# Kernel optimization log

Measured on AMD Instinct MI355X. Metric: run time of the kernel, lower is better.

## Reference

```python
import jax, jax.numpy as jnp
import numpy as np

B, L, C, H, V = 64, 512, 256, 4, 32000
D = C // H
DIL = (1, 2, 4)
WIN = 3
NC = (50, 20)
NEG = -1e9


def setup_inputs() -> dict:
    key = jax.random.key(0)
    ks = jax.random.split(key, 20)
    g = lambda i, shape: jax.random.normal(ks[i], shape, jnp.float32) * 0.05
    Lay = len(DIL)
    x = jax.random.randint(ks[0], (B, L), 0, V)
    emb = g(1, (V, C)).at[0].set(0.0)  # padding_idx=0 row is zero
    return dict(
        x=x, emb=emb, pos=g(2, (L, C)),
        gp_W=g(3, (Lay, C, C)), gp_as=g(4, (Lay, H, D)), gp_ad=g(5, (Lay, H, D)),
        gf_W=g(6, (Lay, C, C)), gf_as=g(7, (Lay, H, D)), gf_ad=g(8, (Lay, H, D)),
        msg_W=g(9, (Lay, C, 2 * C)), msg_b=jnp.zeros((Lay, C), jnp.float32),
        gru_Wih=g(10, (Lay, 3 * C, C)), gru_bih=jnp.zeros((Lay, 3 * C), jnp.float32),
        gru_Whh=g(11, (Lay, 3 * C, C)), gru_bhh=jnp.zeros((Lay, 3 * C), jnp.float32),
        ln_g=jnp.ones((Lay, C), jnp.float32), ln_b=jnp.zeros((Lay, C), jnp.float32),
        pool_w=g(12, (C,)), pool_b=jnp.zeros((), jnp.float32),
        h0_W=g(13, (NC[0], C)), h0_b=jnp.zeros((NC[0],), jnp.float32),
        h1_W=g(14, (NC[1], C)), h1_b=jnp.zeros((NC[1],), jnp.float32),
    )


def _dense_gat(x, W, a_src, a_dst, adj):
    # x: [B,L,C], W: [C_out,C_in], a_*: [H,D], adj: [B,L,L] bool
    b, l, _ = x.shape
    h = jnp.einsum('blc,oc->blo', x, W).reshape(b, l, H, D).transpose(0, 2, 1, 3)  # [B,H,L,D]
    s = jnp.einsum('bhld,hd->bhl', h, a_src)
    d = jnp.einsum('bhld,hd->bhl', h, a_dst)
    e = s[:, :, :, None] + d[:, :, None, :]            # [B,H,L,L]
    e = jnp.where(e > 0, e, 0.2 * e)                   # LeakyReLU(0.2)
    e = jnp.where(adj[:, None, :, :], e, NEG)
    alpha = jax.nn.softmax(e, axis=-1)                 # dropout is identity in eval
    out = jnp.einsum('bhij,bhjd->bhid', alpha, h)
    return out.transpose(0, 2, 1, 3).reshape(b, l, C)


def _forward(x, emb, pos, gp_W, gp_as, gp_ad, gf_W, gf_as, gf_ad,
             msg_W, msg_b, gru_Wih, gru_bih, gru_Whh, gru_bhh,
             ln_g, ln_b, pool_w, pool_b, h0_W, h0_b, h1_W, h1_b):
    mask = x != 0                                      # [B,L]
    mf = mask.astype(jnp.float32)[..., None]           # [B,L,1]
    h = (emb[x] + pos[None, :, :] * mf) * mf
    logical = jnp.clip(jnp.cumsum(mask.astype(jnp.int32), axis=1) - 1, 0)
    valid = mask[:, None, :] & mask[:, :, None]        # [B,L,L]
    eye = jnp.eye(L, dtype=bool)[None]
    for l in range(len(DIL)):
        dil = DIL[l]
        diff = logical[:, :, None] - logical[:, None, :]
        ad = jnp.abs(diff)
        in_win = (ad <= WIN * dil) & (ad % dil == 0)
        adj_p = (valid & in_win & (diff < 0)) | eye
        adj_f = (valid & in_win & (diff > 0)) | eye
        m_p = _dense_gat(h, gp_W[l], gp_as[l], gp_ad[l], adj_p)
        m_f = _dense_gat(h, gf_W[l], gf_as[l], gf_ad[l], adj_f)
        m = jnp.concatenate([m_p, m_f], axis=-1)
        m = jax.nn.relu(jnp.einsum('blk,ck->blc', m, msg_W[l]) + msg_b[l])
        # GRUCell(input=m, hidden=h), PyTorch gate order: r,z,n
        gi = jnp.einsum('blc,gc->blg', m, gru_Wih[l]) + gru_bih[l]
        gh = jnp.einsum('blc,gc->blg', h, gru_Whh[l]) + gru_bhh[l]
        ir, iz, inn = jnp.split(gi, 3, axis=-1)
        hr, hz, hn = jnp.split(gh, 3, axis=-1)
        r = jax.nn.sigmoid(ir + hr)
        z = jax.nn.sigmoid(iz + hz)
        n = jnp.tanh(inn + r * hn)
        h_new = (1.0 - z) * n + z * h
        mu = jnp.mean(h_new, axis=-1, keepdims=True)
        var = jnp.mean(jnp.square(h_new - mu), axis=-1, keepdims=True)
        h_new = (h_new - mu) * jax.lax.rsqrt(var + 1e-5) * ln_g[l] + ln_b[l]
        h = h_new * mf
    # attention pooling over sequence (masked softmax on linear scores)
    sc = jnp.einsum('blc,c->bl', h, pool_w) + pool_b
    sc = jnp.where(mask, sc, NEG)
    a = jax.nn.softmax(sc, axis=-1)
    pooled = jnp.einsum('bl,blc->bc', a, h)            # dropout identity in eval
    o0 = pooled @ h0_W.T + h0_b
    o1 = pooled @ h1_W.T + h1_b
    return jnp.concatenate([o0, o1], axis=-1)          # [B, 50+20]


def reference(x, emb, pos, gp_W, gp_as, gp_ad, gf_W, gf_as, gf_ad,
              msg_W, msg_b, gru_Wih, gru_bih, gru_Whh, gru_bhh,
              ln_g, ln_b, pool_w, pool_b, h0_W, h0_b, h1_W, h1_b):
    return _forward(x, emb, pos, gp_W, gp_as, gp_ad, gf_W, gf_as, gf_ad,
                    msg_W, msg_b, gru_Wih, gru_bih, gru_Whh, gru_bhh,
                    ln_g, ln_b, pool_w, pool_b, h0_W, h0_b, h1_W, h1_b)
```

## Files before the change

kernel.cpp:

```cpp
#include <hip/hip_runtime.h>
#include <math.h>

#define B_ 64
#define L_ 512
#define C_ 256
#define H_ 4
#define LAY 3
#define NEGV -1e9f

#define GF_BIAS  1
#define GF_RELU  2
#define GF_OBF16 4

typedef __attribute__((ext_vector_type(8))) short short8;
typedef __attribute__((ext_vector_type(4))) short short4v;
typedef __attribute__((ext_vector_type(4))) float floatx4;

static __device__ __forceinline__ float rcp_(float x) { return __builtin_amdgcn_rcpf(x); }
static __device__ __forceinline__ float sig_(float x) { return rcp_(1.f + __expf(-x)); }
static __device__ __forceinline__ float tanh_(float x) {
    float e = __expf(2.f * x);
    return 1.f - 2.f * rcp_(e + 1.f);
}

static __device__ __forceinline__ short f2bf(float f) {
    unsigned x = __float_as_uint(f);
    x += 0x7fffu + ((x >> 16) & 1u);
    return (short)(x >> 16);
}
static __device__ __forceinline__ float bf2f(short s) {
    return __uint_as_float(((unsigned)(unsigned short)s) << 16);
}

static __device__ __forceinline__ int tok_swizzle(int blk) {
    int c8 = blk & 7, i = blk >> 3;
    return (c8 + 8 * (i >> 5)) * 128 + (i & 31) * 4;
}

static __device__ __forceinline__ void gl_lds16(const short* g, short* l) {
    __builtin_amdgcn_global_load_lds(
        (const __attribute__((address_space(1))) unsigned int*)g,
        (__attribute__((address_space(3))) unsigned int*)l, 16, 0, 0);
}

__global__ void scan_kernel(const int* __restrict__ x, int* __restrict__ mask,
                            int* __restrict__ logical, int* __restrict__ pol,
                            int* __restrict__ nvalid) {
    int b = blockIdx.x, t = threadIdx.x;
    __shared__ int s[L_];
    int m = (x[b * L_ + t] != 0) ? 1 : 0;
    s[t] = m;
    __syncthreads();
    for (int off = 1; off < L_; off <<= 1) {
        int v = (t >= off) ? s[t - off] : 0;
        __syncthreads();
        s[t] += v;
        __syncthreads();
    }
    int cum = s[t];
    int lg = cum - 1; if (lg < 0) lg = 0;
    mask[b * L_ + t] = m;
    logical[b * L_ + t] = lg;
    if (m) pol[b * L_ + lg] = t;
    if (t == L_ - 1) nvalid[b] = cum;
}

__global__ void embed_kernel(const int* __restrict__ x, const float* __restrict__ emb,
                             const float* __restrict__ pos, short* __restrict__ hb) {
    int t = threadIdx.x;
    int bl = tok_swizzle(blockIdx.x) + (t >> 6);
    int lane = t & 63;
    int xv = x[bl];
    float mf = (xv != 0) ? 1.f : 0.f;
    int l = bl & (L_ - 1);
    float4 e = *(const float4*)&emb[(size_t)xv * C_ + lane * 4];
    float4 p = *(const float4*)&pos[(size_t)l * C_ + lane * 4];
    short4v hv4;
    hv4.x = f2bf((e.x + p.x * mf) * mf);
    hv4.y = f2bf((e.y + p.y * mf) * mf);
    hv4.z = f2bf((e.z + p.z * mf) * mf);
    hv4.w = f2bf((e.w + p.w * mf) * mf);
    *(short4v*)&hb[(size_t)bl * C_ + lane * 4] = hv4;
}

__global__ void f2bf_kernel(const float* __restrict__ s, short* __restrict__ d, int n) {
    int i = blockIdx.x * 256 + threadIdx.x;
    if (i < n) d[i] = f2bf(s[i]);
}

__global__ void prep_wcomb(const float* __restrict__ gpW, const float* __restrict__ gfW,
                           const float* __restrict__ gpas, const float* __restrict__ gpad,
                           const float* __restrict__ gfas, const float* __restrict__ gfad,
                           short* __restrict__ Wc) {
    int i = blockIdx.x * 256 + threadIdx.x;
    if (i >= 3 * 640 * 256) return;
    int k = i & 255;
    int r = (i >> 8) % 640;
    int l = i / (640 * 256);
    float v = 0.f;
    if (r < 256) {
        v = gpW[((size_t)l * 256 + r) * 256 + k];
    } else if (r < 512) {
        v = gfW[((size_t)l * 256 + (r - 256)) * 256 + k];
    } else {
        int n = r - 512;
        if (n < 16) {
            int type = n >> 3, dir = (n >> 2) & 1, hh = n & 3;
            const float* a = type ? (dir ? gfad : gpad) : (dir ? gfas : gpas);
            const float* W = dir ? gfW : gpW;
            for (int j = 0; j < 64; j++) {
                float av = a[l * 256 + hh * 64 + j];
                float wv = W[((size_t)l * 256 + hh * 64 + j) * 256 + k];
                v = fmaf(av, wv, v);
            }
        }
    }
    Wc[i] = f2bf(v);
}

__global__ void prep_gru_i(const float* __restrict__ Wih, const float* __restrict__ Whh,
                           short* __restrict__ Bc) {
    int i = blockIdx.x * 256 + threadIdx.x;
    if (i >= 3 * 1024 * 512) return;
    int k = i & 511, np = (i >> 9) & 1023, l = i >> 19;
    int ch = np >> 2, g = np & 3;
    float v = 0.f;
    if (g < 2) {
        v = (k < 256) ? Wih[((size_t)l * 768 + g * 256 + ch) * 256 + k]
                      : Whh[((size_t)l * 768 + g * 256 + ch) * 256 + (k - 256)];
    } else if (g == 2) {
        if (k < 256) v = Wih[((size_t)l * 768 + 512 + ch) * 256 + k];
    } else {
        if (k >= 256) v = Whh[((size_t)l * 768 + 512 + ch) * 256 + (k - 256)];
    }
    Bc[i] = f2bf(v);
}

__global__ void prep_bias4(const float* __restrict__ bih, const float* __restrict__ bhh,
                           float* __restrict__ bc) {
    int i = blockIdx.x * 256 + threadIdx.x;
    if (i >= 3 * 1024) return;
    int np = i & 1023, l = i >> 10;
    int ch = np >> 2, g = np & 3;
    float v;
    if (g < 2)       v = bih[l * 768 + g * 256 + ch] + bhh[l * 768 + g * 256 + ch];
    else if (g == 2) v = bih[l * 768 + 512 + ch];
    else             v = bhh[l * 768 + 512 + ch];
    bc[i] = v;
}

__global__ __launch_bounds__(256) void bgemm(const short* __restrict__ A0,
                                             const short* __restrict__ Bw,
                                             void* __restrict__ Cout,
                                             const float* __restrict__ bias,
                                             int K, int lda, int ldc, int nstore,
                                             int cbBits, int flags) {
    __shared__ short As[128 * 32];
    __shared__ short Bs[128 * 32];
    const int id = blockIdx.x;
    const int cb = (id >> 3) & ((1 << cbBits) - 1);
    const int rb = (id & 7) + ((id >> (3 + cbBits)) << 3);
    const int tid = threadIdx.x;
    const int wave = tid >> 6, lane = tid & 63;
    const int wm = wave >> 1, wn = wave & 1;
    const size_t arow0 = (size_t)rb * 128;
    const short* Bb = Bw + (size_t)cb * 128 * K;
    floatx4 acc[4][4];
#pragma unroll
    for (int i = 0; i < 4; i++)
#pragma unroll
        for (int j = 0; j < 4; j++) acc[i][j] = (floatx4)0.f;

    const int srow = lane >> 2;
    const int sq = (lane & 3) * 8;
    const int q = lane >> 4, t16 = lane & 15;

    for (int k0 = 0; k0 < K; k0 += 32) {
        const short* Abase = A0 + arow0 * (size_t)lda + k0;
#pragma unroll
        for (int t = 0; t < 2; ++t) {
            int r = (wave * 2 + t) * 16 + srow;
            gl_lds16(Abase + (size_t)r * lda + sq, &As[r * 32 + sq]);
            gl_lds16(Bb + (size_t)r * K + k0 + sq, &Bs[r * 32 + sq]);
        }
        __syncthreads();
        short8 af[4], bfr[4];
#pragma unroll
        for (int mf = 0; mf < 4; mf++)
            af[mf] = *(const short8*)&As[(wm * 64 + mf * 16 + t16) * 32 + q * 8];
#pragma unroll
        for (int nf = 0; nf < 4; nf++)
            bfr[nf] = *(const short8*)&Bs[(wn * 64 + nf * 16 + t16) * 32 + q * 8];
#pragma unroll
        for (int mf = 0; mf < 4; mf++)
#pragma unroll
            for (int nf = 0; nf < 4; nf++)
                acc[nf][mf] = __builtin_amdgcn_mfma_f32_16x16x32_bf16(
                    bfr[nf], af[mf], acc[nf][mf], 0, 0, 0);
        __syncthreads();
    }

    const int rowbase = rb * 128 + wm * 64;
    const int colbase = cb * 128 + wn * 64;
#pragma unroll
    for (int nf = 0; nf < 4; nf++) {
        int col0 = colbase + nf * 16 + q * 4;
        if (col0 >= nstore) continue;
        float4 bv4 = make_float4(0.f, 0.f, 0.f, 0.f);
        if (flags & GF_BIAS) bv4 = *(const float4*)&bias[col0];
#pragma unroll
        for (int mf = 0; mf < 4; mf++) {
            int row = rowbase + mf * 16 + t16;
            float v0 = acc[nf][mf][0] + bv4.x;
            float v1 = acc[nf][mf][1] + bv4.y;
            float v2 = acc[nf][mf][2] + bv4.z;
            float v3 = acc[nf][mf][3] + bv4.w;
            if (flags & GF_RELU) {
                v0 = fmaxf(v0, 0.f); v1 = fmaxf(v1, 0.f);
                v2 = fmaxf(v2, 0.f); v3 = fmaxf(v3, 0.f);
            }
            size_t base = (size_t)row * ldc + col0;
            if (flags & GF_OBF16) {
                short4v pk;
                pk.x = f2bf(v0); pk.y = f2bf(v1); pk.z = f2bf(v2); pk.w = f2bf(v3);
                *(short4v*)&((short*)Cout)[base] = pk;
            } else {
                float4 pk = make_float4(v0, v1, v2, v3);
                *(float4*)&((float*)Cout)[base] = pk;
            }
        }
    }
}

__global__ __launch_bounds__(256) void projssd_bgemm(const short* __restrict__ A0,
                                                     const short* __restrict__ Bw,
                                                     short* __restrict__ hpb2,
                                                     float* __restrict__ Ssd) {
    __shared__ short As[128 * 32];
    __shared__ short Bs[128 * 32];
    const int id = blockIdx.x;
    const int grp = id >> 3;
    const int cb = grp % 5;
    const int rb = (id & 7) + (grp / 5) * 8;
    const int tid = threadIdx.x;
    const int wave = tid >> 6, lane = tid & 63;
    const int wm = wave >> 1, wn = wave & 1;
    const size_t arow0 = (size_t)rb * 128;
    const short* Bb = Bw + (size_t)cb * 128 * 256;
    floatx4 acc[4][4];
#pragma unroll
    for (int i = 0; i < 4; i++)
#pragma unroll
        for (int j = 0; j < 4; j++) acc[i][j] = (floatx4)0.f;

    const int srow = lane >> 2;
    const int sq = (lane & 3) * 8;
    const int q = lane >> 4, t16 = lane & 15;

    for (int k0 = 0; k0 < 256; k0 += 32) {
        const short* Abase = A0 + arow0 * 256 + k0;
#pragma unroll
        for (int t = 0; t < 2; ++t) {
            int r = (wave * 2 + t) * 16 + srow;
            gl_lds16(Abase + (size_t)r * 256 + sq, &As[r * 32 + sq]);
            gl_lds16(Bb + (size_t)r * 256 + k0 + sq, &Bs[r * 32 + sq]);
        }
        __syncthreads();
        short8 af[4], bfr[4];
#pragma unroll
        for (int mf = 0; mf < 4; mf++)
            af[mf] = *(const short8*)&As[(wm * 64 + mf * 16 + t16) * 32 + q * 8];
#pragma unroll
        for (int nf = 0; nf < 4; nf++)
            bfr[nf] = *(const short8*)&Bs[(wn * 64 + nf * 16 + t16) * 32 + q * 8];
#pragma unroll
        for (int mf = 0; mf < 4; mf++)
#pragma unroll
            for (int nf = 0; nf < 4; nf++)
                acc[nf][mf] = __builtin_amdgcn_mfma_f32_16x16x32_bf16(
                    bfr[nf], af[mf], acc[nf][mf], 0, 0, 0);
        __syncthreads();
    }

    const int rowbase = rb * 128 + wm * 64;
    if (cb < 4) {
        const int colbase = cb * 128 + wn * 64;
#pragma unroll
        for (int nf = 0; nf < 4; nf++) {
            int col0 = colbase + nf * 16 + q * 4;
#pragma unroll
            for (int mf = 0; mf < 4; mf++) {
                int row = rowbase + mf * 16 + t16;
                short4v pk;
                pk.x = f2bf(acc[nf][mf][0]);
                pk.y = f2bf(acc[nf][mf][1]);
                pk.z = f2bf(acc[nf][mf][2]);
                pk.w = f2bf(acc[nf][mf][3]);
                *(short4v*)&hpb2[(size_t)row * 512 + col0] = pk;
            }
        }
    } else {
        if (wn == 0) {
            int col0 = q * 4;
            if (col0 < 16) {
#pragma unroll
                for (int mf = 0; mf < 4; mf++) {
                    int row = rowbase + mf * 16 + t16;
                    float4 pk = make_float4(acc[0][mf][0], acc[0][mf][1],
                                            acc[0][mf][2], acc[0][mf][3]);
                    *(float4*)&Ssd[(size_t)row * 16 + col0] = pk;
                }
            }
        }
    }
}

__global__ __launch_bounds__(256) void gru_bgemm(const short* __restrict__ mmb,
                                                 const short* __restrict__ hb_in,
                                                 const short* __restrict__ Bw,
                                                 short* __restrict__ hn2b,
                                                 const float* __restrict__ bias4) {
    __shared__ short As[128 * 36];
    __shared__ short Bs[128 * 32];
    const int id = blockIdx.x;
    const int cb = (id >> 3) & 7;
    const int rb = (id & 7) + ((id >> 6) << 3);
    const int tid = threadIdx.x;
    const int wave = tid >> 6, lane = tid & 63;
    const int wm = wave >> 1, wn = wave & 1;
    const size_t arow0 = (size_t)rb * 128;
    const short* Bb = Bw + (size_t)cb * 128 * 512;
    const int srow = lane >> 2;
    const int sq = (lane & 3) * 8;
    const int q = lane >> 4, t16 = lane & 15;

    floatx4 acc[4][4];
#pragma unroll
    for (int i = 0; i < 4; i++)
#pragma unroll
        for (int j = 0; j < 4; j++) acc[i][j] = (floatx4)0.f;

    for (int k0 = 0; k0 < 512; k0 += 32) {
        const short* Abase = (k0 < 256) ? (mmb + arow0 * 256 + k0)
                                        : (hb_in + arow0 * 256 + (k0 - 256));
#pragma unroll
        for (int t = 0; t < 2; ++t) {
            int r = (wave * 2 + t) * 16 + srow;
            gl_lds16(Abase + (size_t)r * 256 + sq, &As[r * 32 + sq]);
            gl_lds16(Bb + (size_t)r * 512 + k0 + sq, &Bs[r * 32 + sq]);
        }
        __syncthreads();
        short8 af[4], bfr[4];
#pragma unroll
        for (int mf = 0; mf < 4; mf++)
            af[mf] = *(const short8*)&As[(wm * 64 + mf * 16 + t16) * 32 + q * 8];
#pragma unroll
        for (int nf = 0; nf < 4; nf++)
            bfr[nf] = *(const short8*)&Bs[(wn * 64 + nf * 16 + t16) * 32 + q * 8];
#pragma unroll
        for (int mf = 0; mf < 4; mf++)
#pragma unroll
            for (int nf = 0; nf < 4; nf++)
                acc[nf][mf] = __builtin_amdgcn_mfma_f32_16x16x32_bf16(
                    bfr[nf], af[mf], acc[nf][mf], 0, 0, 0);
        __syncthreads();
    }

    float hp[4][4];
#pragma unroll
    for (int nf = 0; nf < 4; nf++) {
        int ch = cb * 32 + wn * 16 + nf * 4 + q;
#pragma unroll
        for (int mf = 0; mf < 4; mf++) {
            int row = rb * 128 + wm * 64 + mf * 16 + t16;
            hp[nf][mf] = bf2f(hb_in[(size_t)row * 256 + ch]);
        }
    }
    const int colbase = cb * 128 + wn * 64;
#pragma unroll
    for (int nf = 0; nf < 4; nf++) {
        int col0 = colbase + nf * 16 + q * 4;
        float4 bv4 = *(const float4*)&bias4[col0];
        int chl = wn * 16 + nf * 4 + q;
#pragma unroll
        for (int mf = 0; mf < 4; mf++) {
            int lrow = wm * 64 + mf * 16 + t16;
            float r = sig_(acc[nf][mf][0] + bv4.x);
            float z = sig_(acc[nf][mf][1] + bv4.y);
            float nv = tanh_((acc[nf][mf][2] + bv4.z) + r * (acc[nf][mf][3] + bv4.w));
            As[lrow * 36 + chl] = f2bf((1.f - z) * nv + z * hp[nf][mf]);
        }
    }
    __syncthreads();
    const int chbase = cb * 32;
#pragma unroll
    for (int it = 0; it < 4; it++) {
        int unit = tid + it * 256;
        int rowl = unit >> 3, ck = unit & 7;
        size_t grow = (size_t)rb * 128 + rowl;
        *(short4v*)&hn2b[grow * 256 + chbase + ck * 4] =
            *(const short4v*)&As[rowl * 36 + ck * 4];
    }
}

__global__ __launch_bounds__(256) void ln_kernel(
    const short* __restrict__ hn2b, short* __restrict__ hb,
    const int* __restrict__ mask,
    const float* __restrict__ lng, const float* __restrict__ lnb) {
    int t = threadIdx.x;
    int bl = tok_swizzle(blockIdx.x) + (t >> 6);
    int lane = t & 63;
    short4v v4 = *(const short4v*)&hn2b[(size_t)bl * C_ + lane * 4];
    float v[4] = {bf2f(v4.x), bf2f(v4.y), bf2f(v4.z), bf2f(v4.w)};
    float s = (v[0] + v[1]) + (v[2] + v[3]);
    float ss = (v[0] * v[0] + v[1] * v[1]) + (v[2] * v[2] + v[3] * v[3]);
#pragma unroll
    for (int off = 32; off; off >>= 1) {
        s += __shfl_xor(s, off);
        ss += __shfl_xor(ss, off);
    }
    float mu = s * (1.f / 256.f);
    float var = ss * (1.f / 256.f) - mu * mu;
    float rstd = rsqrtf(fmaxf(var, 0.f) + 1e-5f);
    float4 lg = *(const float4*)&lng[lane * 4];
    float4 lb = *(const float4*)&lnb[lane * 4];
    float mfv = mask[bl] ? 1.f : 0.f;
    short4v yb;
    yb.x = f2bf(((v[0] - mu) * rstd * lg.x + lb.x) * mfv);
    yb.y = f2bf(((v[1] - mu) * rstd * lg.y + lb.y) * mfv);
    yb.z = f2bf(((v[2] - mu) * rstd * lg.z + lb.z) * mfv);
    yb.w = f2bf(((v[3] - mu) * rstd * lg.w + lb.w) * mfv);
    *(short4v*)&hb[(size_t)bl * C_ + lane * 4] = yb;
}

__global__ __launch_bounds__(256) void agg_fused(
    const short* __restrict__ hpb2, const float* __restrict__ S,
    const int* __restrict__ mask, const int* __restrict__ logical,
    const int* __restrict__ pol, const int* __restrict__ nvalid,
    short* __restrict__ m, int dil) {
    int t = threadIdx.x;
    int bl = tok_swizzle(blockIdx.x) + (t >> 6);
    int sub = t & 63;
    int dir = sub >> 5;
    int slot = sub & 31;
    int cb = slot * 8;
    int head = slot >> 3;
    int b = bl >> 9;

    int mi = mask[bl];
    int li = logical[bl];
    int nv = nvalid[b];
    int js[3]; int nn = 0;
    if (mi) {
#pragma unroll
        for (int k = 1; k <= 3; k++) {
            int lj = dir ? (li - k * dil) : (li + k * dil);
            if (lj >= 0 && lj < nv) js[nn++] = pol[b * L_ + lj];
        }
    }
    int sn = dir * 4 + head, dn = 8 + sn;
    float si = S[(size_t)bl * 16 + sn];
    float di = S[(size_t)bl * 16 + dn];
    float e0 = si + di; e0 = e0 > 0.f ? e0 : 0.2f * e0;
    float emax = e0, ev[3];
    for (int k = 0; k < nn; k++) {
        float djv = S[((size_t)(b * L_ + js[k])) * 16 + dn];
        float e = si + djv; e = e > 0.f ? e : 0.2f * e;
        ev[k] = e; emax = fmaxf(emax, e);
    }
    float w0 = __expf(e0 - emax), den = w0;
    float wv[3];
    for (int k = 0; k < nn; k++) { wv[k] = __expf(ev[k] - emax); den += wv[k]; }
    float rden = rcp_(den);

    size_t base = (size_t)bl * 512 + dir * 256 + cb;
    short8 vself = *(const short8*)&hpb2[base];
    float o[8];
#pragma unroll
    for (int j = 0; j < 8; j++) o[j] = w0 * bf2f(vself[j]);
    for (int k = 0; k < nn; k++) {
        short8 vn = *(const short8*)&hpb2[((size_t)(b * L_ + js[k])) * 512 + dir * 256 + cb];
#pragma unroll
        for (int j = 0; j < 8; j++) o[j] = fmaf(wv[k], bf2f(vn[j]), o[j]);
    }
    short8 ov;
#pragma unroll
    for (int j = 0; j < 8; j++) ov[j] = f2bf(o[j] * rden);
    *(short8*)&m[base] = ov;
}

__global__ __launch_bounds__(1024) void pool_head_kernel(
    const short* __restrict__ hb, const int* __restrict__ mask,
    const float* __restrict__ pw, const float* __restrict__ pb,
    const float* __restrict__ h0W, const float* __restrict__ h0b,
    const float* __restrict__ h1W, const float* __restrict__ h1b,
    float* __restrict__ out) {
    int b = blockIdx.x;
    int t = threadIdx.x;
    int lane = t & 63, wave = t >> 6;
    __shared__ float sc[L_];
    __shared__ float red[20];
    __shared__ float part[4][C_];
    __shared__ float pooled[C_];

    float4 wv = *(const float4*)&pw[lane * 4];
    for (int l = wave; l < L_; l += 16) {
        short4v hv = *(const short4v*)&hb[((size_t)b * L_ + l) * C_ + lane * 4];
        float p = bf2f(hv.x) * wv.x + bf2f(hv.y) * wv.y
                + bf2f(hv.z) * wv.z + bf2f(hv.w) * wv.w;
#pragma unroll
        for (int off = 32; off; off >>= 1) p += __shfl_down(p, off);
        if (lane == 0) sc[l] = mask[b * L_ + l] ? (p + pb[0]) : NEGV;
    }
    __syncthreads();

    float v = (t < L_) ? sc[t] : NEGV;
    float mx = v;
#pragma unroll
    for (int off = 32; off; off >>= 1) mx = fmaxf(mx, __shfl_down(mx, off));
    if (lane == 0) red[wave] = mx;
    __syncthreads();
    if (t == 0) {
        float g = red[0];
        for (int i = 1; i < 16; i++) g = fmaxf(g, red[i]);
        red[16] = g;
    }
    __syncthreads();
    float gmax = red[16];
    float e = (t < L_) ? __expf(v - gmax) : 0.f;
    float ssum = e;
#pragma unroll
    for (int off = 32; off; off >>= 1) ssum += __shfl_down(ssum, off);
    if (lane == 0) red[wave] = ssum;
    __syncthreads();
    if (t == 0) {
        float g = 0.f;
        for (int i = 0; i < 16; i++) g += red[i];
        red[17] = 1.f / g;
    }
    __syncthreads();
    if (t < L_) sc[t] = e * red[17];
    __syncthreads();

    int g = t >> 8, c = t & 255;
    const short* hrow = &hb[((size_t)b * L_ + g * 128) * C_ + c];
    const float* scg = &sc[g * 128];
    float a0 = 0.f, a1 = 0.f, a2 = 0.f, a3 = 0.f;
    for (int l = 0; l < 128; l += 4) {
        a0 = fmaf(scg[l + 0], bf2f(hrow[(size_t)(l + 0) * C_]), a0);
        a1 = fmaf(scg[l + 1], bf2f(hrow[(size_t)(l + 1) * C_]), a1);
        a2 = fmaf(scg[l + 2], bf2f(hrow[(size_t)(l + 2) * C_]), a2);
        a3 = fmaf(scg[l + 3], bf2f(hrow[(size_t)(l + 3) * C_]), a3);
    }
    part[g][c] = (a0 + a1) + (a2 + a3);
    __syncthreads();
    if (t < C_) pooled[t] = (part[0][t] + part[1][t]) + (part[2][t] + part[3][t]);
    __syncthreads();

    for (int o = wave; o < 70; o += 16) {
        const float* W = (o < 50) ? (h0W + (size_t)o * C_) : (h1W + (size_t)(o - 50) * C_);
        float bb = (o < 50) ? h0b[o] : h1b[o - 50];
        float4 w4 = *(const float4*)&W[lane * 4];
        float4 p4 = *(const float4*)&pooled[lane * 4];
        float s = p4.x * w4.x + p4.y * w4.y + p4.z * w4.z + p4.w * w4.w;
#pragma unroll
        for (int off = 32; off; off >>= 1) s += __shfl_down(s, off);
        if (lane == 0) out[b * 70 + o] = s + bb;
    }
}

extern "C" void kernel_launch(void* const* d_in, const int* in_sizes, int n_in,
                              void* d_out, int out_size, void* d_ws, size_t ws_size,
                              hipStream_t stream) {
    const int*   x    = (const int*)d_in[0];
    const float* emb  = (const float*)d_in[1];
    const float* pos  = (const float*)d_in[2];
    const float* gpW  = (const float*)d_in[3];
    const float* gpas = (const float*)d_in[4];
    const float* gpad = (const float*)d_in[5];
    const float* gfW  = (const float*)d_in[6];
    const float* gfas = (const float*)d_in[7];
    const float* gfad = (const float*)d_in[8];
    const float* msgW = (const float*)d_in[9];
    const float* msgb = (const float*)d_in[10];
    const float* Wih  = (const float*)d_in[11];
    const float* bih  = (const float*)d_in[12];
    const float* Whh  = (const float*)d_in[13];
    const float* bhh  = (const float*)d_in[14];
    const float* lng  = (const float*)d_in[15];
    const float* lnb  = (const float*)d_in[16];
    const float* pw   = (const float*)d_in[17];
    const float* pb   = (const float*)d_in[18];
    const float* h0W  = (const float*)d_in[19];
    const float* h0b  = (const float*)d_in[20];
    const float* h1W  = (const float*)d_in[21];
    const float* h1b  = (const float*)d_in[22];
    float* out = (float*)d_out;

    const size_t MW = 1024 * 1024;
    float* ws = (float*)d_ws;
    short* hn2b = (short*)ws;
    short* hb   = (short*)(ws + 8 * MW);
    short* mmb  = (short*)(ws + 12 * MW);
    float* Ssd  = ws + 12 * MW;
    short* hpb2 = (short*)(ws + 16 * MW);
    short* mb   = (short*)(ws + 24 * MW);
    short* Wcomb = (short*)(ws + 32 * MW);
    short* msgWb = Wcomb + 3 * 640 * 256;
    short* Bcat  = msgWb + 3 * 256 * 512;
    float* bias4 = (float*)(Bcat + 3 * 1024 * 512);
    int* mask    = (int*)(bias4 + 3 * 1024);
    int* logical = mask + B_ * L_;
    int* pol     = logical + B_ * L_;
    int* nvalid  = pol + B_ * L_;

    prep_wcomb<<<(3 * 640 * 256 + 255) / 256, 256, 0, stream>>>(gpW, gfW, gpas, gpad,
                                                                gfas, gfad, Wcomb);
    f2bf_kernel<<<(3 * 256 * 512 + 255) / 256, 256, 0, stream>>>(msgW, msgWb, 3 * 256 * 512);
    prep_gru_i<<<(3 * 1024 * 512 + 255) / 256, 256, 0, stream>>>(Wih, Whh, Bcat);
    prep_bias4<<<12, 256, 0, stream>>>(bih, bhh, bias4);

    scan_kernel<<<B_, L_, 0, stream>>>(x, mask, logical, pol, nvalid);
    embed_kernel<<<B_ * L_ / 4, 256, 0, stream>>>(x, emb, pos, hb);

    const int DILS[LAY] = {1, 2, 4};

    for (int l = 0; l < LAY; l++) {
        int dil = DILS[l];
        projssd_bgemm<<<256 * 5, 256, 0, stream>>>(hb, Wcomb + (size_t)l * 640 * 256,
                                                   hpb2, Ssd);
        agg_fused<<<8192, 256, 0, stream>>>(hpb2, Ssd, mask, logical, pol, nvalid, mb, dil);
        bgemm<<<256 * 2, 256, 0, stream>>>(mb, msgWb + (size_t)l * 256 * 512,
                                           mmb, msgb + l * C_, 512, 512, 256, 256, 1,
                                           GF_BIAS | GF_RELU | GF_OBF16);
        gru_bgemm<<<2048, 256, 0, stream>>>(mmb, hb, Bcat + (size_t)l * 1024 * 512,
                                            hn2b, bias4 + l * 1024);
        ln_kernel<<<8192, 256, 0, stream>>>(hn2b, hb, mask, lng + l * C_, lnb + l * C_);
    }

    pool_head_kernel<<<B_, 1024, 0, stream>>>(hb, mask, pw, pb, h0W, h0b, h1W, h1b, out);
}
```

Before: 565.5 us.

## Retile GRU GEMM to 256x256 blocks with double-buffered swizzled LDS pipeline

The fused GRU gate GEMM now uses 256x256 output tiles with 512 threads, a K-step of 64, two LDS buffers that prefetch the next stage while computing, and an XOR-swizzled LDS layout to avoid bank conflicts. Block IDs are also swizzled to group row blocks. The aim is more reuse per global load and overlap of loads with MFMA work, in exchange for fewer blocks (512), heavy accumulator register use and 128KB of LDS per block, which limits occupancy.

```diff
diff --git a/kernel.cpp b/kernel.cpp
--- a/kernel.cpp
+++ b/kernel.cpp
@@ -315,91 +315,120 @@
     }
 }
 
-__global__ __launch_bounds__(256) void gru_bgemm(const short* __restrict__ mmb,
-                                                 const short* __restrict__ hb_in,
-                                                 const short* __restrict__ Bw,
-                                                 short* __restrict__ hn2b,
-                                                 const float* __restrict__ bias4) {
-    __shared__ short As[128 * 36];
-    __shared__ short Bs[128 * 32];
+__global__ __launch_bounds__(512, 2) void gru_bgemm(const short* __restrict__ mmb,
+                                                    const short* __restrict__ hb_in,
+                                                    const short* __restrict__ Bw,
+                                                    short* __restrict__ hn2b,
+                                                    const float* __restrict__ bias4) {
+    __shared__ short lds[2][32768];
     const int id = blockIdx.x;
-    const int cb = (id >> 3) & 7;
-    const int rb = (id & 7) + ((id >> 6) << 3);
+    const int swz = (id & 7) * 64 + (id >> 3);
+    const int rb = swz & 127;
+    const int cb = swz >> 7;
     const int tid = threadIdx.x;
     const int wave = tid >> 6, lane = tid & 63;
-    const int wm = wave >> 1, wn = wave & 1;
-    const size_t arow0 = (size_t)rb * 128;
-    const short* Bb = Bw + (size_t)cb * 128 * 512;
-    const int srow = lane >> 2;
-    const int sq = (lane & 3) * 8;
+    const int wm = wave >> 2, wn = wave & 3;
     const int q = lane >> 4, t16 = lane & 15;
-
-    floatx4 acc[4][4];
+    const size_t arow0 = (size_t)rb * 256;
+    const short* Bb = Bw + (size_t)cb * 256 * 512;
+
+    floatx4 acc[4][8];
 #pragma unroll
     for (int i = 0; i < 4; i++)
 #pragma unroll
-        for (int j = 0; j < 4; j++) acc[i][j] = (floatx4)0.f;
-
-    for (int k0 = 0; k0 < 512; k0 += 32) {
-        const short* Abase = (k0 < 256) ? (mmb + arow0 * 256 + k0)
-                                        : (hb_in + arow0 * 256 + (k0 - 256));
-#pragma unroll
-        for (int t = 0; t < 2; ++t) {
-            int r = (wave * 2 + t) * 16 + srow;
-            gl_lds16(Abase + (size_t)r * 256 + sq, &As[r * 32 + sq]);
-            gl_lds16(Bb + (size_t)r * 512 + k0 + sq, &Bs[r * 32 + sq]);
-        }
-        __syncthreads();
-        short8 af[4], bfr[4];
-#pragma unroll
-        for (int mf = 0; mf < 4; mf++)
-            af[mf] = *(const short8*)&As[(wm * 64 + mf * 16 + t16) * 32 + q * 8];
-#pragma unroll
-        for (int nf = 0; nf < 4; nf++)
-            bfr[nf] = *(const short8*)&Bs[(wn * 64 + nf * 16 + t16) * 32 + q * 8];
-#pragma unroll
-        for (int mf = 0; mf < 4; mf++)
-#pragma unroll
-            for (int nf = 0; nf < 4; nf++)
-                acc[nf][mf] = __builtin_amdgcn_mfma_f32_16x16x32_bf16(
-                    bfr[nf], af[mf], acc[nf][mf], 0, 0, 0);
-        __syncthreads();
-    }
-
-    float hp[4][4];
+        for (int j = 0; j < 8; j++) acc[i][j] = (floatx4)0.f;
+
+    auto stage = [&](int t) {
+        const short* Asrc = (t < 4) ? (mmb + t * 64) : (hb_in + (t * 64 - 256));
+        short* bufA = lds[t & 1];
+        short* bufB = lds[t & 1] + 16384;
+#pragma unroll
+        for (int i = 0; i < 4; ++i) {
+            int unit = i * 512 + tid;
+            int row = unit >> 3;
+            int csw = (unit & 7) ^ (row & 7);
+            gl_lds16(Asrc + (arow0 + (size_t)row) * 256 + csw * 8, bufA + unit * 8);
+        }
+#pragma unroll
+        for (int i = 0; i < 4; ++i) {
+            int unit = i * 512 + tid;
+            int row = unit >> 3;
+            int csw = (unit & 7) ^ (row & 7);
+            gl_lds16(Bb + (size_t)row * 512 + t * 64 + csw * 8, bufB + unit * 8);
+        }
+    };
+
+    auto compute = [&](int t) {
+        const short* bufA = lds[t & 1];
+        const short* bufB = lds[t & 1] + 16384;
+#pragma unroll
+        for (int ks = 0; ks < 2; ++ks) {
+            short8 af[8], bfr[4];
+#pragma unroll
+            for (int mf = 0; mf < 8; mf++) {
+                int row = wm * 128 + mf * 16 + t16;
+                int cg = (ks * 4 + q) ^ (row & 7);
+                af[mf] = *(const short8*)&bufA[row * 64 + cg * 8];
+            }
+#pragma unroll
+            for (int nf = 0; nf < 4; nf++) {
+                int row = wn * 64 + nf * 16 + t16;
+                int cg = (ks * 4 + q) ^ (row & 7);
+                bfr[nf] = *(const short8*)&bufB[row * 64 + cg * 8];
+            }
+            __builtin_amdgcn_s_setprio(1);
+#pragma unroll
+            for (int mf = 0; mf < 8; mf++)
+#pragma unroll
+                for (int nf = 0; nf < 4; nf++)
+                    acc[nf][mf] = __builtin_amdgcn_mfma_f32_16x16x32_bf16(
+                        bfr[nf], af[mf], acc[nf][mf], 0, 0, 0);
+            __builtin_amdgcn_s_setprio(0);
+        }
+    };
+
+    stage(0);
+    stage(1);
+
+    for (int t = 0; t < 7; ++t) {
+        asm volatile("s_waitcnt vmcnt(8)" ::: "memory");
+        __builtin_amdgcn_s_barrier();
+        asm volatile("" ::: "memory");
+        compute(t);
+        asm volatile("" ::: "memory");
+        __builtin_amdgcn_s_barrier();
+        asm volatile("" ::: "memory");
+        if (t < 6) stage(t + 2);
+    }
+    asm volatile("s_waitcnt vmcnt(0)" ::: "memory");
+    __builtin_amdgcn_s_barrier();
+    asm volatile("" ::: "memory");
+    compute(7);
+
+    short* sO = lds[0];
 #pragma unroll
     for (int nf = 0; nf < 4; nf++) {
-        int ch = cb * 32 + wn * 16 + nf * 4 + q;
-#pragma unroll
-        for (int mf = 0; mf < 4; mf++) {
-            int row = rb * 128 + wm * 64 + mf * 16 + t16;
-            hp[nf][mf] = bf2f(hb_in[(size_t)row * 256 + ch]);
-        }
-    }
-    const int colbase = cb * 128 + wn * 64;
-#pragma unroll
-    for (int nf = 0; nf < 4; nf++) {
-        int col0 = colbase + nf * 16 + q * 4;
+        int chl = wn * 16 + nf * 4 + q;
+        int col0 = cb * 256 + wn * 64 + nf * 16 + q * 4;
         float4 bv4 = *(const float4*)&bias4[col0];
-        int chl = wn * 16 + nf * 4 + q;
-#pragma unroll
-        for (int mf = 0; mf < 4; mf++) {
-            int lrow = wm * 64 + mf * 16 + t16;
+#pragma unroll
+        for (int mf = 0; mf < 8; mf++) {
+            int rowl = wm * 128 + mf * 16 + t16;
+            size_t grow = arow0 + rowl;
+            float hp = bf2f(hb_in[grow * 256 + cb * 64 + chl]);
             float r = sig_(acc[nf][mf][0] + bv4.x);
             float z = sig_(acc[nf][mf][1] + bv4.y);
             float nv = tanh_((acc[nf][mf][2] + bv4.z) + r * (acc[nf][mf][3] + bv4.w));
-            As[lrow * 36 + chl] = f2bf((1.f - z) * nv + z * hp[nf][mf]);
-        }
-    }
-    __syncthreads();
-    const int chbase = cb * 32;
-#pragma unroll
-    for (int it = 0; it < 4; it++) {
-        int unit = tid + it * 256;
+            sO[rowl * 72 + chl] = f2bf((1.f - z) * nv + z * hp);
+        }
+    }
+    __syncthreads();
+#pragma unroll
+    for (int it = 0; it < 4; ++it) {
+        int unit = it * 512 + tid;
         int rowl = unit >> 3, ck = unit & 7;
-        size_t grow = (size_t)rb * 128 + rowl;
-        *(short4v*)&hn2b[grow * 256 + chbase + ck * 4] =
-            *(const short4v*)&As[rowl * 36 + ck * 4];
+        *(short8*)&hn2b[(arow0 + rowl) * 256 + cb * 64 + ck * 8] =
+            *(const short8*)&sO[rowl * 72 + ck * 8];
     }
 }
 
@@ -633,8 +662,8 @@
         bgemm<<<256 * 2, 256, 0, stream>>>(mb, msgWb + (size_t)l * 256 * 512,
                                            mmb, msgb + l * C_, 512, 512, 256, 256, 1,
                                            GF_BIAS | GF_RELU | GF_OBF16);
-        gru_bgemm<<<2048, 256, 0, stream>>>(mmb, hb, Bcat + (size_t)l * 1024 * 512,
-                                            hn2b, bias4 + l * 1024);
+        gru_bgemm<<<512, 512, 0, stream>>>(mmb, hb, Bcat + (size_t)l * 1024 * 512,
+                                           hn2b, bias4 + l * 1024);
         ln_kernel<<<8192, 256, 0, stream>>>(hn2b, hb, mask, lng + l * C_, lnb + l * C_);
     }
 
```

Measured after the change: 557.1 us. No clear change (-1.5%).
